# Optimization experiments

Measured on AMD Instinct MI355X. Metric: run time of the kernel, lower is better.

The kernel has to match this reference:

```python
import jax, jax.numpy as jnp
import numpy as np

HEAD_DIM = 64
N_HEADS = 16


def _rope_tables(seq_len, head_dim):
    pos = np.arange(seq_len, dtype=np.float32)
    freq = np.arange(0, head_dim, 2, dtype=np.float32) / head_dim
    inv_freq = 1.0 / (10000.0 ** freq)
    angles = np.outer(pos, inv_freq)                     # [S, D/2]
    angles = np.repeat(angles, 2, axis=-1)               # [S, D] interleaved
    return jnp.asarray(np.cos(angles)), jnp.asarray(np.sin(angles))


def _rotate_half(x):
    x1 = x[..., ::2]
    x2 = x[..., 1::2]
    return jnp.stack((-x2, x1), axis=-1).reshape(x.shape)


def _apply_rope(x, cos, sin):
    # x: [B, H, S, D]; cos/sin: [S, D]
    return x * cos + _rotate_half(x) * sin


def setup_inputs() -> dict:
    key = jax.random.key(0)
    ks = jax.random.split(key, 5)
    d = N_HEADS * HEAD_DIM
    B, S = 4, 2048
    s = 1.0 / np.sqrt(d)
    return {
        "x": jax.random.normal(ks[0], (B, S, d), dtype=jnp.float32),
        "Wq": jax.random.normal(ks[1], (d, d), dtype=jnp.float32) * s,
        "bq": jnp.zeros((d,), jnp.float32),
        "Wk": jax.random.normal(ks[2], (d, d), dtype=jnp.float32) * s,
        "bk": jnp.zeros((d,), jnp.float32),
        "Wv": jax.random.normal(ks[3], (d, d), dtype=jnp.float32) * s,
        "bv": jnp.zeros((d,), jnp.float32),
        "Wo": jax.random.normal(ks[4], (d, d), dtype=jnp.float32) * s,
        "bo": jnp.zeros((d,), jnp.float32),
    }


def reference(x, Wq, bq, Wk, bk, Wv, bv, Wo, bo):
    B, S, d = x.shape
    H, D = N_HEADS, HEAD_DIM
    scale = D ** -0.5

    q = (x @ Wq + bq).reshape(B, S, H, D).transpose(0, 2, 1, 3)  # [B,H,S,D]
    k = (x @ Wk + bk).reshape(B, S, H, D).transpose(0, 2, 1, 3)
    v = (x @ Wv + bv).reshape(B, S, H, D).transpose(0, 2, 1, 3)

    cos, sin = _rope_tables(S, D)
    q = _apply_rope(q, cos, sin)
    k = _apply_rope(k, cos, sin)

    att = jnp.einsum("bhqd,bhkd->bhqk", q, k) * scale            # [B,H,S,S]
    causal = jnp.tril(jnp.ones((S, S), dtype=bool))
    att = jnp.where(causal, att, -jnp.inf)
    att = jax.nn.softmax(att, axis=-1)

    y = jnp.einsum("bhqk,bhkd->bhqd", att, v)                    # [B,H,S,D]
    y = y.transpose(0, 2, 1, 3).reshape(B, S, d)
    return y @ Wo + bo
```

## Files before the change

### kernel.cpp

```cpp
#include <hip/hip_runtime.h>

typedef __bf16 bf16;
typedef __bf16 bf16x2 __attribute__((ext_vector_type(2)));
typedef __bf16 bf16x8 __attribute__((ext_vector_type(8)));
typedef float  f32x4  __attribute__((ext_vector_type(4)));

#define MFMA16(a,b,c) __builtin_amdgcn_mfma_f32_16x16x32_bf16(a,b,c,0,0,0)
#define GLL16(g, l) __builtin_amdgcn_global_load_lds( \
    (const __attribute__((address_space(1))) unsigned char*)(g), \
    (__attribute__((address_space(3))) unsigned char*)(l), 16, 0, 0)

constexpr int SEQ   = 2048;
constexpr int NH    = 16;
constexpr int HD    = 64;
constexpr int BATCH = 4;
constexpr int DM    = 1024;
constexpr int ROWS  = BATCH * SEQ;
constexpr size_t TEN = (size_t)BATCH * NH * SEQ * HD;

__global__ __launch_bounds__(256) void k_prep(const float* __restrict__ x,
                                              const float* __restrict__ W0,
                                              const float* __restrict__ W1,
                                              const float* __restrict__ W2,
                                              const float* __restrict__ W3,
                                              bf16* __restrict__ Wt_all,
                                              bf16* __restrict__ xb) {
    __shared__ float T[64][65];
    const int z = blockIdx.z;
    const int t = threadIdx.x;
    if (z == 4) {
        const int bi = blockIdx.y * 16 + blockIdx.x;
#pragma unroll
        for (int c = 0; c < 16; c++) {
            const size_t idx = (size_t)c * 524288 + ((size_t)bi * 256 + t) * 8;
            float4 f0 = *(const float4*)(x + idx);
            float4 f1 = *(const float4*)(x + idx + 4);
            bf16x8 o;
            o[0] = (bf16)f0.x; o[1] = (bf16)f0.y; o[2] = (bf16)f0.z; o[3] = (bf16)f0.w;
            o[4] = (bf16)f1.x; o[5] = (bf16)f1.y; o[6] = (bf16)f1.z; o[7] = (bf16)f1.w;
            *(bf16x8*)(xb + idx) = o;
        }
        return;
    }
    const float* W = (z == 0) ? W0 : (z == 1) ? W1 : (z == 2) ? W2 : W3;
    bf16* Wt = Wt_all + (size_t)z * DM * DM;
    const int kb = blockIdx.x, nb = blockIdx.y;
    const int rl = t >> 2, seg = t & 3;
    const float* src = W + (size_t)(kb * 64 + rl) * DM + nb * 64 + seg * 16;
#pragma unroll
    for (int j4 = 0; j4 < 4; j4++) {
        float4 f = *(const float4*)(src + j4 * 4);
        T[rl][seg * 16 + j4 * 4 + 0] = f.x;
        T[rl][seg * 16 + j4 * 4 + 1] = f.y;
        T[rl][seg * 16 + j4 * 4 + 2] = f.z;
        T[rl][seg * 16 + j4 * 4 + 3] = f.w;
    }
    __syncthreads();
    bf16* dst = Wt + (size_t)(nb * 64 + rl) * DM + kb * 64 + seg * 16;
    bf16x8 o0, o1;
#pragma unroll
    for (int j = 0; j < 8; j++) {
        o0[j] = (bf16)T[seg * 16 + j][rl];
        o1[j] = (bf16)T[seg * 16 + 8 + j][rl];
    }
    *(bf16x8*)dst = o0;
    *(bf16x8*)(dst + 8) = o1;
}

template <int MODE>
__global__ __launch_bounds__(256) void k_gemm(const bf16* __restrict__ A,
                                              const bf16* __restrict__ Wt0,
                                              const float* __restrict__ b0,
                                              const float* __restrict__ b1,
                                              const float* __restrict__ b2,
                                              void* __restrict__ out) {
    __shared__ __align__(1024) bf16 AsF[128 * 32];
    __shared__ __align__(1024) bf16 BsF[128 * 32];
    const int z = blockIdx.z;
    const bf16* Wt = Wt0 + (size_t)z * DM * DM;
    const float* bias = (z == 0) ? b0 : (z == 1) ? b1 : b2;

    const int t = threadIdx.x;
    const int w = t >> 6, lane = t & 63, quad = lane >> 4, l16 = lane & 15;
    const int bm = blockIdx.x * 128, bn = blockIdx.y * 128;
    const int wm = (w >> 1) * 64, wn = (w & 1) * 64;

    const int c0 = w * 2, c1 = w * 2 + 1;
    const int sg0 = c0 * 64 + lane, sg1 = c1 * 64 + lane;
    const int r0 = sg0 >> 2, r1 = sg1 >> 2;
    const int csg0 = (sg0 & 3) ^ ((r0 >> 1) & 3);
    const int csg1 = (sg1 & 3) ^ ((r1 >> 1) & 3);
    const bf16* gA0 = A  + (size_t)(bm + r0) * DM + csg0 * 8;
    const bf16* gA1 = A  + (size_t)(bm + r1) * DM + csg1 * 8;
    const bf16* gB0 = Wt + (size_t)(bn + r0) * DM + csg0 * 8;
    const bf16* gB1 = Wt + (size_t)(bn + r1) * DM + csg1 * 8;
    bf16* lA0 = AsF + c0 * 512;
    bf16* lA1 = AsF + c1 * 512;
    bf16* lB0 = BsF + c0 * 512;
    bf16* lB1 = BsF + c1 * 512;

    const bf16* pA[4]; const bf16* pB[4];
#pragma unroll
    for (int mt = 0; mt < 4; mt++) {
        const int r = wm + mt * 16 + l16;
        pA[mt] = AsF + r * 32 + ((quad ^ ((r >> 1) & 3)) << 3);
    }
#pragma unroll
    for (int nt = 0; nt < 4; nt++) {
        const int r = wn + nt * 16 + l16;
        pB[nt] = BsF + r * 32 + ((quad ^ ((r >> 1) & 3)) << 3);
    }

    f32x4 zero = {0.f, 0.f, 0.f, 0.f};
    f32x4 acc[4][4];
#pragma unroll
    for (int mt = 0; mt < 4; mt++)
#pragma unroll
        for (int nt = 0; nt < 4; nt++) acc[mt][nt] = zero;

    for (int k0 = 0; k0 < DM; k0 += 32) {
        __syncthreads();
        GLL16(gA0, lA0);
        GLL16(gA1, lA1);
        GLL16(gB0, lB0);
        GLL16(gB1, lB1);
        gA0 += 32; gA1 += 32; gB0 += 32; gB1 += 32;
        __syncthreads();

        bf16x8 af[4], bfr[4];
#pragma unroll
        for (int mt = 0; mt < 4; mt++) af[mt]  = *(const bf16x8*)pA[mt];
#pragma unroll
        for (int nt = 0; nt < 4; nt++) bfr[nt] = *(const bf16x8*)pB[nt];
#pragma unroll
        for (int mt = 0; mt < 4; mt++)
#pragma unroll
            for (int nt = 0; nt < 4; nt++)
                acc[mt][nt] = MFMA16(af[mt], bfr[nt], acc[mt][nt]);
    }

    float bv[4], invf[4];
#pragma unroll
    for (int nt = 0; nt < 4; nt++) {
        const int col = bn + wn + nt * 16 + l16;
        bv[nt] = bias[col];
        if (MODE == 0) {
            const int i = (col & 63) >> 1;
            invf[nt] = __builtin_exp2f(-0.41524101186092029f * (float)i);
        }
    }
    const int odd = l16 & 1;

#pragma unroll
    for (int mt = 0; mt < 4; mt++) {
#pragma unroll
        for (int nt = 0; nt < 4; nt++) {
            const int col = bn + wn + nt * 16 + l16;
#pragma unroll
            for (int rg = 0; rg < 4; rg++) {
                const int row = bm + wm + mt * 16 + quad * 4 + rg;
                float val = acc[mt][nt][rg] + bv[nt];
                if (MODE == 0) {
                    const int b = row >> 11, s = row & (SEQ - 1);
                    const int h = col >> 6, dd = col & 63;
                    if (z < 2) {
                        const float partner = __shfl_xor(val, 1);
                        float sn, cs;
                        __sincosf((float)s * invf[nt], &sn, &cs);
                        val = odd ? (val * cs + partner * sn)
                                  : (val * cs - partner * sn);
                        if (z == 0) val *= 0.125f;
                    }
                    ((bf16*)out)[(size_t)z * TEN +
                                 (((size_t)(b * NH + h)) * SEQ + s) * HD + dd] = (bf16)val;
                } else {
                    ((float*)out)[(size_t)row * DM + col] = val;
                }
            }
        }
    }
}

__global__ __launch_bounds__(256) void k_vtrans(const bf16* __restrict__ v, bf16* __restrict__ vt) {
    __shared__ float T[64][65];
    const int t = threadIdx.x;
    const int sb = blockIdx.x, bh = blockIdx.y;
    const int rl = t >> 2, seg = t & 3;
    const bf16* src = v + ((size_t)bh * SEQ + sb * 64 + rl) * HD + seg * 16;
    bf16x8 i0 = *(const bf16x8*)src;
    bf16x8 i1 = *(const bf16x8*)(src + 8);
#pragma unroll
    for (int j = 0; j < 8; j++) {
        T[rl][seg * 16 + j]     = (float)i0[j];
        T[rl][seg * 16 + 8 + j] = (float)i1[j];
    }
    __syncthreads();
    bf16* dst = vt + ((size_t)bh * HD + rl) * SEQ + sb * 64 + seg * 16;
    bf16x8 o0, o1;
#pragma unroll
    for (int j = 0; j < 8; j++) {
        o0[j] = (bf16)T[seg * 16 + j][rl];
        o1[j] = (bf16)T[seg * 16 + 8 + j][rl];
    }
    *(bf16x8*)dst = o0;
    *(bf16x8*)(dst + 8) = o1;
}

__global__ __launch_bounds__(256, 2) void k_attn(const bf16* __restrict__ q,
                                                 const bf16* __restrict__ k,
                                                 const bf16* __restrict__ vt,
                                                 bf16* __restrict__ y) {
    __shared__ __align__(1024) bf16 KsF[64 * 64];
    __shared__ __align__(1024) bf16 VsF[64 * 64];
    __shared__ __align__(1024) bf16 PsF[4 * 32 * 64];
    const int t = threadIdx.x;
    const int w = t >> 6, lane = t & 63, quad = lane >> 4, l16 = lane & 15;
    const int bh = blockIdx.x;
    const int qb = 15 - (int)blockIdx.y;
    const int b = bh >> 4, h = bh & 15;

    const int srow = lane >> 3;
    const int gseg = (lane & 7) ^ srow;
    const int c0 = w, c1 = w + 4;

    const bf16* kbase = k  + (size_t)bh * SEQ * HD;
    const bf16* vbase = vt + (size_t)bh * HD * SEQ;
    const float NEG_INF = -__builtin_inff();

    const bf16 *kf_p[4][2], *vf_p[4][2], *pf_p[2][2];
#pragma unroll
    for (int nt = 0; nt < 4; nt++) {
        const int r = nt * 16 + l16;
#pragma unroll
        for (int hh = 0; hh < 2; hh++) {
            const int sg = hh * 4 + quad;
            kf_p[nt][hh] = KsF + r * 64 + (((sg ^ (r & 7))) << 3);
            vf_p[nt][hh] = VsF + r * 64 + (((sg ^ (r & 7))) << 3);
        }
    }
#pragma unroll
    for (int mt = 0; mt < 2; mt++) {
        const int r = mt * 16 + l16;
#pragma unroll
        for (int hh = 0; hh < 2; hh++) {
            const int sg = hh * 4 + quad;
            pf_p[mt][hh] = PsF + w * 2048 + r * 64 + (((sg ^ (r & 7))) << 3);
        }
    }

    bf16x8 qf[2][2];
#pragma unroll
    for (int mt = 0; mt < 2; mt++) {
        const bf16* qrow = q + ((size_t)bh * SEQ + qb * 128 + w * 32 + mt * 16 + l16) * HD;
        qf[mt][0] = *(const bf16x8*)(qrow + quad * 8);
        qf[mt][1] = *(const bf16x8*)(qrow + 32 + quad * 8);
    }

    f32x4 zero = {0.f, 0.f, 0.f, 0.f};
    f32x4 minus10 = {-10.f, -10.f, -10.f, -10.f};
    f32x4 acc_o[2][4];
    float l_acc[2][4];
#pragma unroll
    for (int mt = 0; mt < 2; mt++)
#pragma unroll
        for (int nt = 0; nt < 4; nt++) acc_o[mt][nt] = zero;
#pragma unroll
    for (int mt = 0; mt < 2; mt++)
#pragma unroll
        for (int rg = 0; rg < 4; rg++) l_acc[mt][rg] = 0.f;

    const bf16* kg0 = kbase + (size_t)(c0 * 8 + srow) * HD + gseg * 8;
    const bf16* kg1 = kbase + (size_t)(c1 * 8 + srow) * HD + gseg * 8;
    const bf16* vg0 = vbase + (size_t)(c0 * 8 + srow) * SEQ + gseg * 8;
    const bf16* vg1 = vbase + (size_t)(c1 * 8 + srow) * SEQ + gseg * 8;
    const int ktmax = 2 * qb + 1;

    for (int kt = 0; kt <= ktmax; kt++) {
        __syncthreads();
        GLL16(kg0, KsF + c0 * 512);
        GLL16(kg1, KsF + c1 * 512);
        GLL16(vg0, VsF + c0 * 512);
        GLL16(vg1, VsF + c1 * 512);
        kg0 += 64 * HD; kg1 += 64 * HD; vg0 += 64; vg1 += 64;
        __syncthreads();

        const int d = qb * 128 + w * 32 - kt * 64;
        if (d > -32) {
            f32x4 accs[2][4];
#pragma unroll
            for (int nt = 0; nt < 4; nt++) {
                const bf16x8 kf0 = *(const bf16x8*)kf_p[nt][0];
                const bf16x8 kf1 = *(const bf16x8*)kf_p[nt][1];
#pragma unroll
                for (int mt = 0; mt < 2; mt++) {
                    f32x4 a = minus10;
                    a = MFMA16(qf[mt][0], kf0, a);
                    a = MFMA16(qf[mt][1], kf1, a);
                    accs[mt][nt] = a;
                }
            }
            if (d < 64) {
#pragma unroll
                for (int mt = 0; mt < 2; mt++) {
                    const int qr = d + mt * 16 + quad * 4;
#pragma unroll
                    for (int nt = 0; nt < 4; nt++) {
                        const int kv = nt * 16 + l16;
#pragma unroll
                        for (int rg = 0; rg < 4; rg++)
                            if (kv > qr + rg) accs[mt][nt][rg] = NEG_INF;
                    }
                }
            }
#pragma unroll
            for (int mt = 0; mt < 2; mt++) {
#pragma unroll
                for (int nt = 0; nt < 4; nt++) {
#pragma unroll
                    for (int rg = 0; rg < 4; rg++) {
                        const float p = __expf(accs[mt][nt][rg]);
                        l_acc[mt][rg] += p;
                        const int prow = mt * 16 + quad * 4 + rg;
                        const int psg  = (nt * 2 + (l16 >> 3)) ^ (prow & 7);
                        PsF[w * 2048 + prow * 64 + psg * 8 + (l16 & 7)] = (bf16)p;
                    }
                }
            }
            bf16x8 pf[2][2];
#pragma unroll
            for (int mt = 0; mt < 2; mt++) {
                pf[mt][0] = *(const bf16x8*)pf_p[mt][0];
                pf[mt][1] = *(const bf16x8*)pf_p[mt][1];
            }
#pragma unroll
            for (int nt = 0; nt < 4; nt++) {
                const bf16x8 vf0 = *(const bf16x8*)vf_p[nt][0];
                const bf16x8 vf1 = *(const bf16x8*)vf_p[nt][1];
#pragma unroll
                for (int mt = 0; mt < 2; mt++) {
                    acc_o[mt][nt] = MFMA16(pf[mt][0], vf0, acc_o[mt][nt]);
                    acc_o[mt][nt] = MFMA16(pf[mt][1], vf1, acc_o[mt][nt]);
                }
            }
        }
    }

#pragma unroll
    for (int mt = 0; mt < 2; mt++) {
#pragma unroll
        for (int rg = 0; rg < 4; rg++) {
            float rs = l_acc[mt][rg];
            rs += __shfl_xor(rs, 1);
            rs += __shfl_xor(rs, 2);
            rs += __shfl_xor(rs, 4);
            rs += __shfl_xor(rs, 8);
            const float inv = 1.0f / rs;
            const int s = qb * 128 + w * 32 + mt * 16 + quad * 4 + rg;
#pragma unroll
            for (int nt = 0; nt < 4; nt++) {
                const float val = acc_o[mt][nt][rg] * inv;
                y[((size_t)(b * SEQ + s)) * DM + h * HD + nt * 16 + l16] = (bf16)val;
            }
        }
    }
}

extern "C" void kernel_launch(void* const* d_in, const int* in_sizes, int n_in,
                              void* d_out, int out_size, void* d_ws, size_t ws_size,
                              hipStream_t stream) {
    const float* x  = (const float*)d_in[0];
    const float* Wq = (const float*)d_in[1];
    const float* bq = (const float*)d_in[2];
    const float* Wk = (const float*)d_in[3];
    const float* bk = (const float*)d_in[4];
    const float* Wv = (const float*)d_in[5];
    const float* bv = (const float*)d_in[6];
    const float* Wo = (const float*)d_in[7];
    const float* bo = (const float*)d_in[8];

    char* ws = (char*)d_ws;
    bf16* xb   = (bf16*)(ws);
    bf16* wall = (bf16*)(ws + (16ull << 20));
    bf16* qb   = (bf16*)(ws + (24ull << 20));
    bf16* kb   = (bf16*)(ws + (40ull << 20));
    bf16* vb   = (bf16*)(ws + (56ull << 20));
    bf16* vtb  = (bf16*)(ws + (72ull << 20));
    bf16* wot  = wall + 3ull * DM * DM;

    k_prep<<<dim3(16, 16, 5), 256, 0, stream>>>(x, Wq, Wk, Wv, Wo, wall, xb);
    k_gemm<0><<<dim3(64, 8, 3), 256, 0, stream>>>(xb, wall, bq, bk, bv, qb);
    k_vtrans<<<dim3(32, 64), 256, 0, stream>>>(vb, vtb);
    k_attn<<<dim3(64, 16), 256, 0, stream>>>(qb, kb, vtb, xb);
    k_gemm<1><<<dim3(64, 8, 1), 256, 0, stream>>>(xb, wot, bo, bo, bo, d_out);
}
```

Before: 255.1 us.

## Replace QKV projection GEMM with 256x256-tile pipelined 8-wave kernel

Adds a dedicated QKV projection kernel that uses 256x256 output tiles, 512 threads, and a double-buffered LDS staging scheme with XOR-swizzled layout. Global-to-LDS loads for upcoming k-tiles are interleaved with MFMA phases under explicit barriers, waitcnt drains and priority raising. The generic GEMM keeps only the output-projection path. The aim is more data reuse per tile and better overlap of memory loads with matrix math. In exchange it adds register pressure and fragile hand-scheduled synchronisation, and with 384 blocks it may not fill the device evenly.

```diff
diff --git a/kernel.cpp b/kernel.cpp
--- a/kernel.cpp
+++ b/kernel.cpp
@@ -9,6 +9,8 @@
 #define GLL16(g, l) __builtin_amdgcn_global_load_lds( \
     (const __attribute__((address_space(1))) unsigned char*)(g), \
     (__attribute__((address_space(3))) unsigned char*)(l), 16, 0, 0)
+#define BARRIER() asm volatile("s_barrier" ::: "memory")
+#define DRAIN(n)  asm volatile("s_waitcnt vmcnt(" #n ")" ::: "memory")
 
 constexpr int SEQ   = 2048;
 constexpr int NH    = 16;
@@ -65,6 +67,144 @@
     }
     *(bf16x8*)dst = o0;
     *(bf16x8*)(dst + 8) = o1;
+}
+
+__global__ __launch_bounds__(512, 2) void k_qkv(const bf16* __restrict__ A,
+                                                const bf16* __restrict__ Wt0,
+                                                const float* __restrict__ b0,
+                                                const float* __restrict__ b1,
+                                                const float* __restrict__ b2,
+                                                bf16* __restrict__ out) {
+    __shared__ __align__(1024) bf16 Lds[8 * 8192];
+    const int t = threadIdx.x;
+    const int w = t >> 6, lane = t & 63, quad = lane >> 4, l16 = lane & 15;
+    const int bm  = blockIdx.x * 256;
+    const int by  = blockIdx.y;
+    const int z   = by >> 2;
+    const int bnl = (by & 3) * 256;
+    const bf16* Wt = Wt0 + (size_t)z * DM * DM;
+    const float* bias = (z == 0) ? b0 : (z == 1) ? b1 : b2;
+
+    const int srow = lane >> 3;
+    const int sseg = (lane & 7) ^ srow;
+    const bf16* gA = A  + (size_t)(bm  + w * 8 + srow) * DM + sseg * 8;
+    const bf16* gB = Wt + (size_t)(bnl + w * 8 + srow) * DM + sseg * 8;
+
+#define SLOT(buf, mat, half) ((((buf) * 2 + (mat)) * 2 + (half)) * 8192)
+#define STG(mat, buf, half, tIdx) do { \
+    const bf16* _g = ((mat) ? gB : gA) + (size_t)(half) * 128 * DM + (size_t)(tIdx) * 64; \
+    bf16* _l = Lds + SLOT(buf, mat, half) + w * 512; \
+    GLL16(_g, _l); \
+    GLL16(_g + 64 * DM, _l + 4096); \
+} while (0)
+
+    const int s0 = quad ^ (l16 & 7);
+    const int s1 = (4 + quad) ^ (l16 & 7);
+    const int aoff0 = l16 * 64 + (s0 << 3);
+    const int aoff1 = l16 * 64 + (s1 << 3);
+    const int brow  = (w & 1) * 64 + l16;
+    const int boff0 = brow * 64 + (s0 << 3);
+    const int boff1 = brow * 64 + (s1 << 3);
+    const int AB0 = SLOT(0, 0, w >> 2),       AB1 = SLOT(1, 0, w >> 2);
+    const int BB0 = SLOT(0, 1, (w >> 1) & 1), BB1 = SLOT(1, 1, (w >> 1) & 1);
+
+    f32x4 zero = {0.f, 0.f, 0.f, 0.f};
+    f32x4 acc[8][4];
+#pragma unroll
+    for (int mt = 0; mt < 8; mt++)
+#pragma unroll
+        for (int nt = 0; nt < 4; nt++) acc[mt][nt] = zero;
+    bf16x8 bfr[4][2];
+
+#define PHASE(ABx, BBx, P, DRAIN_STMT, ...) do { \
+    if ((P) == 0) { \
+        _Pragma("unroll") \
+        for (int nt = 0; nt < 4; nt++) { \
+            bfr[nt][0] = *(const bf16x8*)(Lds + (BBx) + nt * 1024 + boff0); \
+            bfr[nt][1] = *(const bf16x8*)(Lds + (BBx) + nt * 1024 + boff1); \
+        } \
+    } \
+    bf16x8 af[2][2]; \
+    _Pragma("unroll") \
+    for (int mi = 0; mi < 2; mi++) { \
+        af[mi][0] = *(const bf16x8*)(Lds + (ABx) + (2 * (P) + mi) * 1024 + aoff0); \
+        af[mi][1] = *(const bf16x8*)(Lds + (ABx) + (2 * (P) + mi) * 1024 + aoff1); \
+    } \
+    __VA_ARGS__; \
+    DRAIN_STMT; \
+    BARRIER(); \
+    __builtin_amdgcn_s_setprio(1); \
+    _Pragma("unroll") \
+    for (int mi = 0; mi < 2; mi++) \
+        _Pragma("unroll") \
+        for (int nt = 0; nt < 4; nt++) { \
+            f32x4 a = acc[2 * (P) + mi][nt]; \
+            a = MFMA16(af[mi][0], bfr[nt][0], a); \
+            a = MFMA16(af[mi][1], bfr[nt][1], a); \
+            acc[2 * (P) + mi][nt] = a; \
+        } \
+    __builtin_amdgcn_s_setprio(0); \
+    BARRIER(); \
+} while (0)
+
+    STG(1, 0, 0, 0); STG(1, 0, 1, 0);
+    STG(0, 0, 0, 0); STG(0, 0, 1, 0);
+    STG(1, 1, 0, 1); STG(1, 1, 1, 1);
+    DRAIN(0);
+    BARRIER();
+
+    for (int i = 0; i < 8; i++) {
+        const int tO1 = 2 * i + 1;
+        const int tE  = (i < 7) ? 2 * i + 2 : 15;
+        const int tO2 = (i < 7) ? 2 * i + 3 : 15;
+        PHASE(AB0, BB0, 0, , STG(0, 1, 0, tO1); STG(0, 1, 1, tO1));
+        PHASE(AB0, BB0, 1, , STG(1, 0, 0, tE));
+        PHASE(AB0, BB0, 2, , STG(1, 0, 1, tE));
+        PHASE(AB0, BB0, 3, DRAIN(4), );
+        PHASE(AB1, BB1, 0, , STG(0, 0, 0, tE); STG(0, 0, 1, tE));
+        PHASE(AB1, BB1, 1, , STG(1, 1, 0, tO2));
+        PHASE(AB1, BB1, 2, , STG(1, 1, 1, tO2));
+        PHASE(AB1, BB1, 3, DRAIN(4), );
+    }
+#undef PHASE
+#undef STG
+#undef SLOT
+
+    const int wml = (w >> 2) * 128;
+    const int wnl = (w & 3) * 64;
+    float bv[4], invf[4];
+#pragma unroll
+    for (int nt = 0; nt < 4; nt++) {
+        const int colz = bnl + wnl + nt * 16 + l16;
+        bv[nt] = bias[colz];
+        const int ip = (colz & 63) >> 1;
+        invf[nt] = __builtin_exp2f(-0.41524101186092029f * (float)ip);
+    }
+    const int odd = l16 & 1;
+#pragma unroll
+    for (int mt = 0; mt < 8; mt++) {
+#pragma unroll
+        for (int nt = 0; nt < 4; nt++) {
+            const int colz = bnl + wnl + nt * 16 + l16;
+            const int h = colz >> 6, dd = colz & 63;
+#pragma unroll
+            for (int rg = 0; rg < 4; rg++) {
+                const int row = bm + wml + mt * 16 + quad * 4 + rg;
+                float val = acc[mt][nt][rg] + bv[nt];
+                const int b = row >> 11, s = row & (SEQ - 1);
+                if (z < 2) {
+                    const float partner = __shfl_xor(val, 1);
+                    float sn, cs;
+                    __sincosf((float)s * invf[nt], &sn, &cs);
+                    val = odd ? (val * cs + partner * sn)
+                              : (val * cs - partner * sn);
+                    if (z == 0) val *= 0.125f;
+                }
+                out[(size_t)z * TEN +
+                    (((size_t)(b * NH + h)) * SEQ + s) * HD + dd] = (bf16)val;
+            }
+        }
+    }
 }
 
 template <int MODE>
@@ -139,17 +279,12 @@
                 acc[mt][nt] = MFMA16(af[mt], bfr[nt], acc[mt][nt]);
     }
 
-    float bv[4], invf[4];
+    float bv[4];
 #pragma unroll
     for (int nt = 0; nt < 4; nt++) {
         const int col = bn + wn + nt * 16 + l16;
         bv[nt] = bias[col];
-        if (MODE == 0) {
-            const int i = (col & 63) >> 1;
-            invf[nt] = __builtin_exp2f(-0.41524101186092029f * (float)i);
-        }
-    }
-    const int odd = l16 & 1;
+    }
 
 #pragma unroll
     for (int mt = 0; mt < 4; mt++) {
@@ -160,22 +295,7 @@
             for (int rg = 0; rg < 4; rg++) {
                 const int row = bm + wm + mt * 16 + quad * 4 + rg;
                 float val = acc[mt][nt][rg] + bv[nt];
-                if (MODE == 0) {
-                    const int b = row >> 11, s = row & (SEQ - 1);
-                    const int h = col >> 6, dd = col & 63;
-                    if (z < 2) {
-                        const float partner = __shfl_xor(val, 1);
-                        float sn, cs;
-                        __sincosf((float)s * invf[nt], &sn, &cs);
-                        val = odd ? (val * cs + partner * sn)
-                                  : (val * cs - partner * sn);
-                        if (z == 0) val *= 0.125f;
-                    }
-                    ((bf16*)out)[(size_t)z * TEN +
-                                 (((size_t)(b * NH + h)) * SEQ + s) * HD + dd] = (bf16)val;
-                } else {
-                    ((float*)out)[(size_t)row * DM + col] = val;
-                }
+                ((float*)out)[(size_t)row * DM + col] = val;
             }
         }
     }
@@ -388,7 +508,7 @@
     bf16* wot  = wall + 3ull * DM * DM;
 
     k_prep<<<dim3(16, 16, 5), 256, 0, stream>>>(x, Wq, Wk, Wv, Wo, wall, xb);
-    k_gemm<0><<<dim3(64, 8, 3), 256, 0, stream>>>(xb, wall, bq, bk, bv, qb);
+    k_qkv<<<dim3(32, 12), 512, 0, stream>>>(xb, wall, bq, bk, bv, qb);
     k_vtrans<<<dim3(32, 64), 256, 0, stream>>>(vb, vtb);
     k_attn<<<dim3(64, 16), 256, 0, stream>>>(qb, kb, vtb, xb);
     k_gemm<1><<<dim3(64, 8, 1), 256, 0, stream>>>(xb, wot, bo, bo, bo, d_out);
```

After: 257.1 us. About the same (+0.8%).

## Triple-buffer GEMM and attention loads; write transposed V from GEMM epilogue

Applied to the files above, without the earlier changes.

Replaces the two-barrier synchronous load loops in the projection GEMM and attention kernels with a three-stage LDS ring. Global-to-LDS copies for tile k+2 are issued while tile k is computed, and only a vmcnt wait plus one barrier runs per iteration. The V projection now writes its output directly in transposed [B,H,D,S] layout from the GEMM epilogue, which removes the separate transpose kernel and its extra global round trip. The cost is three times the LDS per block, which may lower occupancy. The raw s_waitcnt and s_barrier asm also depends on the exact count of outstanding loads.

```diff
diff --git a/kernel.cpp b/kernel.cpp
--- a/kernel.cpp
+++ b/kernel.cpp
@@ -2,6 +2,7 @@
 
 typedef __bf16 bf16;
 typedef __bf16 bf16x2 __attribute__((ext_vector_type(2)));
+typedef __bf16 bf16x4 __attribute__((ext_vector_type(4)));
 typedef __bf16 bf16x8 __attribute__((ext_vector_type(8)));
 typedef float  f32x4  __attribute__((ext_vector_type(4)));
 
@@ -9,6 +10,8 @@
 #define GLL16(g, l) __builtin_amdgcn_global_load_lds( \
     (const __attribute__((address_space(1))) unsigned char*)(g), \
     (__attribute__((address_space(3))) unsigned char*)(l), 16, 0, 0)
+#define BARRIER() asm volatile("s_barrier" ::: "memory")
+#define DRAIN(n)  asm volatile("s_waitcnt vmcnt(" #n ")" ::: "memory")
 
 constexpr int SEQ   = 2048;
 constexpr int NH    = 16;
@@ -68,14 +71,15 @@
 }
 
 template <int MODE>
-__global__ __launch_bounds__(256) void k_gemm(const bf16* __restrict__ A,
-                                              const bf16* __restrict__ Wt0,
-                                              const float* __restrict__ b0,
-                                              const float* __restrict__ b1,
-                                              const float* __restrict__ b2,
-                                              void* __restrict__ out) {
-    __shared__ __align__(1024) bf16 AsF[128 * 32];
-    __shared__ __align__(1024) bf16 BsF[128 * 32];
+__global__ __launch_bounds__(256, 3) void k_gemm(const bf16* __restrict__ A,
+                                                 const bf16* __restrict__ Wt0,
+                                                 const float* __restrict__ b0,
+                                                 const float* __restrict__ b1,
+                                                 const float* __restrict__ b2,
+                                                 bf16* __restrict__ vt,
+                                                 void* __restrict__ out) {
+    __shared__ __align__(1024) bf16 AsF[3][4096];
+    __shared__ __align__(1024) bf16 BsF[3][4096];
     const int z = blockIdx.z;
     const bf16* Wt = Wt0 + (size_t)z * DM * DM;
     const float* bias = (z == 0) ? b0 : (z == 1) ? b1 : b2;
@@ -94,21 +98,27 @@
     const bf16* gA1 = A  + (size_t)(bm + r1) * DM + csg1 * 8;
     const bf16* gB0 = Wt + (size_t)(bn + r0) * DM + csg0 * 8;
     const bf16* gB1 = Wt + (size_t)(bn + r1) * DM + csg1 * 8;
-    bf16* lA0 = AsF + c0 * 512;
-    bf16* lA1 = AsF + c1 * 512;
-    bf16* lB0 = BsF + c0 * 512;
-    bf16* lB1 = BsF + c1 * 512;
-
-    const bf16* pA[4]; const bf16* pB[4];
+
+#define STG(buf, tt) do { \
+    GLL16(gA0 + (size_t)(tt) * 32, &AsF[buf][c0 * 512]); \
+    GLL16(gA1 + (size_t)(tt) * 32, &AsF[buf][c1 * 512]); \
+    GLL16(gB0 + (size_t)(tt) * 32, &BsF[buf][c0 * 512]); \
+    GLL16(gB1 + (size_t)(tt) * 32, &BsF[buf][c1 * 512]); \
+} while (0)
+
+    STG(0, 0);
+    STG(1, 1);
+
+    int offA[4], offB[4];
 #pragma unroll
     for (int mt = 0; mt < 4; mt++) {
         const int r = wm + mt * 16 + l16;
-        pA[mt] = AsF + r * 32 + ((quad ^ ((r >> 1) & 3)) << 3);
+        offA[mt] = r * 32 + ((quad ^ ((r >> 1) & 3)) << 3);
     }
 #pragma unroll
     for (int nt = 0; nt < 4; nt++) {
         const int r = wn + nt * 16 + l16;
-        pB[nt] = BsF + r * 32 + ((quad ^ ((r >> 1) & 3)) << 3);
+        offB[nt] = r * 32 + ((quad ^ ((r >> 1) & 3)) << 3);
     }
 
     f32x4 zero = {0.f, 0.f, 0.f, 0.f};
@@ -118,26 +128,35 @@
 #pragma unroll
         for (int nt = 0; nt < 4; nt++) acc[mt][nt] = zero;
 
-    for (int k0 = 0; k0 < DM; k0 += 32) {
-        __syncthreads();
-        GLL16(gA0, lA0);
-        GLL16(gA1, lA1);
-        GLL16(gB0, lB0);
-        GLL16(gB1, lB1);
-        gA0 += 32; gA1 += 32; gB0 += 32; gB1 += 32;
-        __syncthreads();
-
+    DRAIN(4);
+    BARRIER();
+
+#pragma unroll
+    for (int tk = 0; tk < 32; tk++) {
+        const int cur = tk % 3;
+        if (tk < 31) {
+            const int nb = (tk + 2) % 3;
+            const int ts = (tk + 2 > 31) ? 31 : (tk + 2);
+            STG(nb, ts);
+        }
+        const bf16* ab = &AsF[cur][0];
+        const bf16* bb = &BsF[cur][0];
         bf16x8 af[4], bfr[4];
 #pragma unroll
-        for (int mt = 0; mt < 4; mt++) af[mt]  = *(const bf16x8*)pA[mt];
-#pragma unroll
-        for (int nt = 0; nt < 4; nt++) bfr[nt] = *(const bf16x8*)pB[nt];
+        for (int mt = 0; mt < 4; mt++) af[mt]  = *(const bf16x8*)(ab + offA[mt]);
+#pragma unroll
+        for (int nt = 0; nt < 4; nt++) bfr[nt] = *(const bf16x8*)(bb + offB[nt]);
 #pragma unroll
         for (int mt = 0; mt < 4; mt++)
 #pragma unroll
             for (int nt = 0; nt < 4; nt++)
                 acc[mt][nt] = MFMA16(af[mt], bfr[nt], acc[mt][nt]);
-    }
+        if (tk < 31) {
+            DRAIN(4);
+            BARRIER();
+        }
+    }
+#undef STG
 
     float bv[4], invf[4];
 #pragma unroll
@@ -151,6 +170,24 @@
     }
     const int odd = l16 & 1;
 
+    if (MODE == 0 && z == 2) {
+#pragma unroll
+        for (int mt = 0; mt < 4; mt++) {
+            const int row0 = bm + wm + mt * 16 + quad * 4;
+            const int b = row0 >> 11, s0 = row0 & (SEQ - 1);
+#pragma unroll
+            for (int nt = 0; nt < 4; nt++) {
+                const int col = bn + wn + nt * 16 + l16;
+                const int h = col >> 6, dd = col & 63;
+                bf16x4 o;
+#pragma unroll
+                for (int rg = 0; rg < 4; rg++) o[rg] = (bf16)(acc[mt][nt][rg] + bv[nt]);
+                *(bf16x4*)(vt + ((size_t)((b * NH + h) * HD + dd)) * SEQ + s0) = o;
+            }
+        }
+        return;
+    }
+
 #pragma unroll
     for (int mt = 0; mt < 4; mt++) {
 #pragma unroll
@@ -163,14 +200,12 @@
                 if (MODE == 0) {
                     const int b = row >> 11, s = row & (SEQ - 1);
                     const int h = col >> 6, dd = col & 63;
-                    if (z < 2) {
-                        const float partner = __shfl_xor(val, 1);
-                        float sn, cs;
-                        __sincosf((float)s * invf[nt], &sn, &cs);
-                        val = odd ? (val * cs + partner * sn)
-                                  : (val * cs - partner * sn);
-                        if (z == 0) val *= 0.125f;
-                    }
+                    const float partner = __shfl_xor(val, 1);
+                    float sn, cs;
+                    __sincosf((float)s * invf[nt], &sn, &cs);
+                    val = odd ? (val * cs + partner * sn)
+                              : (val * cs - partner * sn);
+                    if (z == 0) val *= 0.125f;
                     ((bf16*)out)[(size_t)z * TEN +
                                  (((size_t)(b * NH + h)) * SEQ + s) * HD + dd] = (bf16)val;
                 } else {
@@ -181,37 +216,12 @@
     }
 }
 
-__global__ __launch_bounds__(256) void k_vtrans(const bf16* __restrict__ v, bf16* __restrict__ vt) {
-    __shared__ float T[64][65];
-    const int t = threadIdx.x;
-    const int sb = blockIdx.x, bh = blockIdx.y;
-    const int rl = t >> 2, seg = t & 3;
-    const bf16* src = v + ((size_t)bh * SEQ + sb * 64 + rl) * HD + seg * 16;
-    bf16x8 i0 = *(const bf16x8*)src;
-    bf16x8 i1 = *(const bf16x8*)(src + 8);
-#pragma unroll
-    for (int j = 0; j < 8; j++) {
-        T[rl][seg * 16 + j]     = (float)i0[j];
-        T[rl][seg * 16 + 8 + j] = (float)i1[j];
-    }
-    __syncthreads();
-    bf16* dst = vt + ((size_t)bh * HD + rl) * SEQ + sb * 64 + seg * 16;
-    bf16x8 o0, o1;
-#pragma unroll
-    for (int j = 0; j < 8; j++) {
-        o0[j] = (bf16)T[seg * 16 + j][rl];
-        o1[j] = (bf16)T[seg * 16 + 8 + j][rl];
-    }
-    *(bf16x8*)dst = o0;
-    *(bf16x8*)(dst + 8) = o1;
-}
-
 __global__ __launch_bounds__(256, 2) void k_attn(const bf16* __restrict__ q,
                                                  const bf16* __restrict__ k,
                                                  const bf16* __restrict__ vt,
                                                  bf16* __restrict__ y) {
-    __shared__ __align__(1024) bf16 KsF[64 * 64];
-    __shared__ __align__(1024) bf16 VsF[64 * 64];
+    __shared__ __align__(1024) bf16 KsF[3][4096];
+    __shared__ __align__(1024) bf16 VsF[3][4096];
     __shared__ __align__(1024) bf16 PsF[4 * 32 * 64];
     const int t = threadIdx.x;
     const int w = t >> 6, lane = t & 63, quad = lane >> 4, l16 = lane & 15;
@@ -227,26 +237,17 @@
     const bf16* vbase = vt + (size_t)bh * HD * SEQ;
     const float NEG_INF = -__builtin_inff();
 
-    const bf16 *kf_p[4][2], *vf_p[4][2], *pf_p[2][2];
-#pragma unroll
-    for (int nt = 0; nt < 4; nt++) {
-        const int r = nt * 16 + l16;
-#pragma unroll
-        for (int hh = 0; hh < 2; hh++) {
-            const int sg = hh * 4 + quad;
-            kf_p[nt][hh] = KsF + r * 64 + (((sg ^ (r & 7))) << 3);
-            vf_p[nt][hh] = VsF + r * 64 + (((sg ^ (r & 7))) << 3);
-        }
-    }
-#pragma unroll
-    for (int mt = 0; mt < 2; mt++) {
-        const int r = mt * 16 + l16;
-#pragma unroll
-        for (int hh = 0; hh < 2; hh++) {
-            const int sg = hh * 4 + quad;
-            pf_p[mt][hh] = PsF + w * 2048 + r * 64 + (((sg ^ (r & 7))) << 3);
-        }
-    }
+    const int koff0 = (c0 * 8 + srow) * HD + gseg * 8;
+    const int koff1 = (c1 * 8 + srow) * HD + gseg * 8;
+    const int voff0 = (c0 * 8 + srow) * SEQ + gseg * 8;
+    const int voff1 = (c1 * 8 + srow) * SEQ + gseg * 8;
+
+#define STGKV(buf, tt) do { \
+    GLL16(kbase + (size_t)(tt) * 64 * HD + koff0, &KsF[buf][c0 * 512]); \
+    GLL16(kbase + (size_t)(tt) * 64 * HD + koff1, &KsF[buf][c1 * 512]); \
+    GLL16(vbase + (size_t)(tt) * 64 + voff0, &VsF[buf][c0 * 512]); \
+    GLL16(vbase + (size_t)(tt) * 64 + voff1, &VsF[buf][c1 * 512]); \
+} while (0)
 
     bf16x8 qf[2][2];
 #pragma unroll
@@ -256,6 +257,31 @@
         qf[mt][1] = *(const bf16x8*)(qrow + 32 + quad * 8);
     }
 
+    const int ktmax = 2 * qb + 1;
+    STGKV(0, 0);
+    STGKV(1, 1);
+
+    int off_kv[4][2];
+#pragma unroll
+    for (int nt = 0; nt < 4; nt++) {
+        const int r = nt * 16 + l16;
+#pragma unroll
+        for (int hh = 0; hh < 2; hh++) {
+            const int sg = hh * 4 + quad;
+            off_kv[nt][hh] = r * 64 + ((sg ^ (r & 7)) << 3);
+        }
+    }
+    const bf16 *pf_p[2][2];
+#pragma unroll
+    for (int mt = 0; mt < 2; mt++) {
+        const int r = mt * 16 + l16;
+#pragma unroll
+        for (int hh = 0; hh < 2; hh++) {
+            const int sg = hh * 4 + quad;
+            pf_p[mt][hh] = PsF + w * 2048 + r * 64 + ((sg ^ (r & 7)) << 3);
+        }
+    }
+
     f32x4 zero = {0.f, 0.f, 0.f, 0.f};
     f32x4 minus10 = {-10.f, -10.f, -10.f, -10.f};
     f32x4 acc_o[2][4];
@@ -269,28 +295,25 @@
 #pragma unroll
         for (int rg = 0; rg < 4; rg++) l_acc[mt][rg] = 0.f;
 
-    const bf16* kg0 = kbase + (size_t)(c0 * 8 + srow) * HD + gseg * 8;
-    const bf16* kg1 = kbase + (size_t)(c1 * 8 + srow) * HD + gseg * 8;
-    const bf16* vg0 = vbase + (size_t)(c0 * 8 + srow) * SEQ + gseg * 8;
-    const bf16* vg1 = vbase + (size_t)(c1 * 8 + srow) * SEQ + gseg * 8;
-    const int ktmax = 2 * qb + 1;
-
+    DRAIN(4);
+    BARRIER();
+
+    int cur = 0, nb = 2;
     for (int kt = 0; kt <= ktmax; kt++) {
-        __syncthreads();
-        GLL16(kg0, KsF + c0 * 512);
-        GLL16(kg1, KsF + c1 * 512);
-        GLL16(vg0, VsF + c0 * 512);
-        GLL16(vg1, VsF + c1 * 512);
-        kg0 += 64 * HD; kg1 += 64 * HD; vg0 += 64; vg1 += 64;
-        __syncthreads();
+        if (kt < ktmax) {
+            const int ts = (kt + 2 > ktmax) ? ktmax : (kt + 2);
+            STGKV(nb, ts);
+        }
+        const bf16* kb_ = &KsF[0][0] + cur * 4096;
+        const bf16* vb_ = &VsF[0][0] + cur * 4096;
 
         const int d = qb * 128 + w * 32 - kt * 64;
         if (d > -32) {
             f32x4 accs[2][4];
 #pragma unroll
             for (int nt = 0; nt < 4; nt++) {
-                const bf16x8 kf0 = *(const bf16x8*)kf_p[nt][0];
-                const bf16x8 kf1 = *(const bf16x8*)kf_p[nt][1];
+                const bf16x8 kf0 = *(const bf16x8*)(kb_ + off_kv[nt][0]);
+                const bf16x8 kf1 = *(const bf16x8*)(kb_ + off_kv[nt][1]);
 #pragma unroll
                 for (int mt = 0; mt < 2; mt++) {
                     f32x4 a = minus10;
@@ -334,8 +357,8 @@
             }
 #pragma unroll
             for (int nt = 0; nt < 4; nt++) {
-                const bf16x8 vf0 = *(const bf16x8*)vf_p[nt][0];
-                const bf16x8 vf1 = *(const bf16x8*)vf_p[nt][1];
+                const bf16x8 vf0 = *(const bf16x8*)(vb_ + off_kv[nt][0]);
+                const bf16x8 vf1 = *(const bf16x8*)(vb_ + off_kv[nt][1]);
 #pragma unroll
                 for (int mt = 0; mt < 2; mt++) {
                     acc_o[mt][nt] = MFMA16(pf[mt][0], vf0, acc_o[mt][nt]);
@@ -343,7 +366,14 @@
                 }
             }
         }
-    }
+        if (kt < ktmax) {
+            DRAIN(4);
+            BARRIER();
+        }
+        cur = (cur == 2) ? 0 : cur + 1;
+        nb  = (nb  == 2) ? 0 : nb  + 1;
+    }
+#undef STGKV
 
 #pragma unroll
     for (int mt = 0; mt < 2; mt++) {
@@ -383,13 +413,11 @@
     bf16* wall = (bf16*)(ws + (16ull << 20));
     bf16* qb   = (bf16*)(ws + (24ull << 20));
     bf16* kb   = (bf16*)(ws + (40ull << 20));
-    bf16* vb   = (bf16*)(ws + (56ull << 20));
     bf16* vtb  = (bf16*)(ws + (72ull << 20));
     bf16* wot  = wall + 3ull * DM * DM;
 
     k_prep<<<dim3(16, 16, 5), 256, 0, stream>>>(x, Wq, Wk, Wv, Wo, wall, xb);
-    k_gemm<0><<<dim3(64, 8, 3), 256, 0, stream>>>(xb, wall, bq, bk, bv, qb);
-    k_vtrans<<<dim3(32, 64), 256, 0, stream>>>(vb, vtb);
+    k_gemm<0><<<dim3(64, 8, 3), 256, 0, stream>>>(xb, wall, bq, bk, bv, vtb, qb);
     k_attn<<<dim3(64, 16), 256, 0, stream>>>(qb, kb, vtb, xb);
-    k_gemm<1><<<dim3(64, 8, 1), 256, 0, stream>>>(xb, wot, bo, bo, bo, d_out);
+    k_gemm<1><<<dim3(64, 8, 1), 256, 0, stream>>>(xb, wot, bo, bo, bo, vtb, d_out);
 }
```

Result: no change. 253.7 us (-0.5%).
